# Kernel tuning notes

Hardware: AMD Instinct MI355X
Metric: run time of the kernel (lower is better)

## Reference

```python
import jax, jax.numpy as jnp
import numpy as np

R_BLOCKS = 8  # r: number of diagonal blocks

def _rotate(Wp, R):
    # Wp: [out, in], R: [r, b, b] with in = r*b.
    # Equivalent to Wp @ block_diag(R[0],...,R[r-1]) without materializing [in,in].
    o = Wp.shape[0]
    r, b, _ = R.shape
    Wb = Wp.reshape(o, r, b)
    return jnp.einsum('ori,rij->orj', Wb, R).reshape(o, r * b)

def setup_inputs() -> dict:
    key = jax.random.key(0)
    ks = jax.random.split(key, 6)
    in_f, out_f, r = 1024, 1024, R_BLOCKS
    blk = in_f // r
    return {
        'attn': jax.random.normal(ks[0], (3 * out_f, in_f), jnp.float32) * 0.02,
        'bias': jax.random.normal(ks[1], (3 * out_f,), jnp.float32) * 0.02,
        'x': jax.random.normal(ks[2], (4, 2048, in_f), jnp.float32),
        'q_R': jax.random.normal(ks[3], (r, blk, blk), jnp.float32) * 0.02,
        'k_R': jax.random.normal(ks[4], (r, blk, blk), jnp.float32) * 0.02,
        'v_R': jax.random.normal(ks[5], (r, blk, blk), jnp.float32) * 0.02,
    }

def reference(attn, bias, x, q_R, k_R, v_R):
    # attn.data in torch detaches the frozen pretrained weight
    W = jax.lax.stop_gradient(attn)
    Wq, Wk, Wv = jnp.split(W, 3, axis=0)
    filt = jnp.concatenate([_rotate(Wq, q_R), _rotate(Wk, k_R), _rotate(Wv, v_R)], axis=0)
    # F.linear: x @ filt.T + bias -> [B, S, 3*out]
    return jnp.einsum('bsi,oi->bso', x, filt) + bias
```

## Files before the change

### kernel.cpp

```cpp
#include <hip/hip_runtime.h>
#include <hip/hip_bf16.h>
#include <stdint.h>

typedef __attribute__((ext_vector_type(8))) short short8;
typedef __attribute__((ext_vector_type(4))) float floatx4;

#define M_TOT 8192
#define N_TOT 3072
#define K_TOT 1024

__device__ inline unsigned short f2bf(float f) {
    union { float f; unsigned int ui; } v; v.f = f;
    unsigned int x = v.ui;
    unsigned int r = (x + 0x7fffu + ((x >> 16) & 1u)) >> 16;
    return (unsigned short)r;
}

__device__ inline void gl2lds16(const void* g, void* l) {
    __builtin_amdgcn_global_load_lds(
        (__attribute__((address_space(1))) void*)g,
        (__attribute__((address_space(3))) void*)l,
        16, 0, 0);
}

__global__ __launch_bounds__(256) void cvt_f32_bf16_kernel(
    const float* __restrict__ in, unsigned short* __restrict__ out, int n8)
{
    int i = blockIdx.x * 256 + threadIdx.x;
    if (i >= n8) return;
    const float4* p = (const float4*)in + (size_t)i * 2;
    float4 a = p[0], b = p[1];
    short8 s;
    s[0] = (short)f2bf(a.x); s[1] = (short)f2bf(a.y);
    s[2] = (short)f2bf(a.z); s[3] = (short)f2bf(a.w);
    s[4] = (short)f2bf(b.x); s[5] = (short)f2bf(b.y);
    s[6] = (short)f2bf(b.z); s[7] = (short)f2bf(b.w);
    *(short8*)(out + (size_t)i * 8) = s;
}

__global__ __launch_bounds__(256) void rotate_w_kernel(
    const float* __restrict__ W,
    const float* __restrict__ qR,
    const float* __restrict__ kR,
    const float* __restrict__ vR,
    unsigned short* __restrict__ Fout)
{
    __shared__ float Rs[128 * 128];
    __shared__ float Ws[64 * 132];

    const int tid = threadIdx.x;
    const int o0 = blockIdx.x * 64;
    const int r = blockIdx.y;

    const float* R = (o0 < 1024) ? qR : (o0 < 2048) ? kR : vR;
    R += (size_t)r * 128 * 128;

#pragma unroll
    for (int i = 0; i < 16; ++i) {
        int idx = (i * 256 + tid) * 4;
        *(float4*)(Rs + idx) = *(const float4*)(R + idx);
    }
#pragma unroll
    for (int i = 0; i < 8; ++i) {
        int idx = (i * 256 + tid) * 4;
        int row = idx >> 7;
        int col = idx & 127;
        *(float4*)(Ws + row * 132 + col) =
            *(const float4*)(W + (size_t)(o0 + row) * K_TOT + r * 128 + col);
    }
    __syncthreads();

    const int jg = (tid & 15) * 8;
    const int ob = tid >> 4;

    float acc[4][8];
#pragma unroll
    for (int a = 0; a < 4; ++a)
#pragma unroll
        for (int b = 0; b < 8; ++b) acc[a][b] = 0.f;

    for (int i = 0; i < 128; ++i) {
        float4 r0 = *(const float4*)(Rs + i * 128 + jg);
        float4 r1 = *(const float4*)(Rs + i * 128 + jg + 4);
        float rv[8] = {r0.x, r0.y, r0.z, r0.w, r1.x, r1.y, r1.z, r1.w};
#pragma unroll
        for (int oo = 0; oo < 4; ++oo) {
            float wv = Ws[(ob + oo * 16) * 132 + i];
#pragma unroll
            for (int t = 0; t < 8; ++t) acc[oo][t] += wv * rv[t];
        }
    }

#pragma unroll
    for (int oo = 0; oo < 4; ++oo) {
        int o = o0 + ob + oo * 16;
        short8 s;
#pragma unroll
        for (int t = 0; t < 8; ++t) s[t] = (short)f2bf(acc[oo][t]);
        *(short8*)(Fout + (size_t)o * K_TOT + r * 128 + jg) = s;
    }
}

#define GKT 16

__global__ __launch_bounds__(512, 2) void gemm256_kernel(
    const unsigned short* __restrict__ X,
    const unsigned short* __restrict__ F,
    const float* __restrict__ bias,
    float* __restrict__ out)
{
    extern __shared__ unsigned short sm[];

    const int tid = threadIdx.x;
    const int wid = tid >> 6;
    const int l   = tid & 63;
    const int wm  = wid >> 2;
    const int wn  = wid & 3;

    const int bswz = (blockIdx.x & 7) * 48 + (blockIdx.x >> 3);
    const int m0 = (bswz / 12) * 256;
    const int n0 = (bswz % 12) * 256;

    const int srow  = tid >> 3;
    const int scb   = tid & 7;
    const int sgcb  = scb ^ (srow & 7);
    const int sswap = (tid >> 8) << 5;

    const unsigned short* Xs = X + (size_t)(m0 + srow) * K_TOT + sgcb * 8;
    const unsigned short* Fs = F + (size_t)(n0 + srow + sswap) * K_TOT + sgcb * 8;
    unsigned short* smA = sm + srow * 64 + scb * 8;
    unsigned short* smB = sm + 32768 + (srow + sswap) * 64 + scb * 8;

#define STAGE_A(bo, rb, kc) gl2lds16(Xs + (size_t)(rb) * K_TOT + (kc), smA + (bo) + (rb) * 64)
#define STAGE_B(bo, rb, kc) gl2lds16(Fs + (size_t)(rb) * K_TOT + (kc), smB + (bo) + (rb) * 64)
#define STAGE_Ag0(bo, kc) { STAGE_A(bo, 0, kc);  STAGE_A(bo, 128, kc); }
#define STAGE_Ag1(bo, kc) { STAGE_A(bo, 64, kc); STAGE_A(bo, 192, kc); }
#define STAGE_Bg0(bo, kc) { STAGE_B(bo, 0, kc);  STAGE_B(bo, 128, kc); }
#define STAGE_Bg1(bo, kc) { STAGE_B(bo, 32, kc); STAGE_B(bo, 160, kc); }
#define BARRIER() asm volatile("s_barrier" ::: "memory")

    const int l15 = l & 15;
    const int s8a = (((l >> 4) + 0) ^ (l & 7)) * 8;
    const int s8b = (((l >> 4) + 4) ^ (l & 7)) * 8;
    const int paBase = (wm * 128 + l15) * 64;
    const int pbBase = (wn * 64 + l15) * 64;

    floatx4 acc[8][4];
#pragma unroll
    for (int i = 0; i < 8; ++i)
#pragma unroll
        for (int j = 0; j < 4; ++j)
#pragma unroll
            for (int t = 0; t < 4; ++t) acc[i][j][t] = 0.f;

    short8 aF[4][2];
    short8 bF[2][2][2];

#define RD_A(QM, co) { _Pragma("unroll") for (int mf = 0; mf < 4; ++mf) { \
        const unsigned short* p = sm + (co) + paBase + ((QM) * 4 + mf) * 1024; \
        aF[mf][0] = *(const short8*)(p + s8a); \
        aF[mf][1] = *(const short8*)(p + s8b); } }
#define RD_B(QN, co) { _Pragma("unroll") for (int nf = 0; nf < 2; ++nf) { \
        const unsigned short* p = sm + 32768 + (co) + pbBase + ((QN) * 2 + nf) * 1024; \
        bF[QN][nf][0] = *(const short8*)(p + s8a); \
        bF[QN][nf][1] = *(const short8*)(p + s8b); } }
#define DO_MFMA(QM, QN) { __builtin_amdgcn_s_setprio(1); \
        _Pragma("unroll") for (int mf = 0; mf < 4; ++mf) \
        _Pragma("unroll") for (int nf = 0; nf < 2; ++nf) { \
            acc[(QM)*4+mf][(QN)*2+nf] = __builtin_amdgcn_mfma_f32_16x16x32_bf16( \
                aF[mf][0], bF[QN][nf][0], acc[(QM)*4+mf][(QN)*2+nf], 0, 0, 0); \
            acc[(QM)*4+mf][(QN)*2+nf] = __builtin_amdgcn_mfma_f32_16x16x32_bf16( \
                aF[mf][1], bF[QN][nf][1], acc[(QM)*4+mf][(QN)*2+nf], 0, 0, 0); } \
        __builtin_amdgcn_s_setprio(0); }

    STAGE_Ag0(0, 0); STAGE_Bg0(0, 0); STAGE_Bg1(0, 0); STAGE_Ag1(0, 0);
    STAGE_Ag0(16384, 64); STAGE_Bg0(16384, 64);
    asm volatile("s_waitcnt vmcnt(4)" ::: "memory");
    BARRIER();

    for (int kt = 0; kt < GKT; ++kt) {
        const int co = (kt & 1) << 14;
        const int no = co ^ 16384;
        const int kc1 = (kt + 1) * 64;
        const int kc2 = (kt + 2) * 64;

        RD_A(0, co); RD_B(0, co);
        if (kt + 1 < GKT) { STAGE_Bg1(no, kc1); }
        BARRIER();
        DO_MFMA(0, 0);
        BARRIER();

        RD_B(1, co);
        if (kt + 1 < GKT) { STAGE_Ag1(no, kc1); }
        BARRIER();
        DO_MFMA(0, 1);
        BARRIER();

        RD_A(1, co);
        if (kt + 2 < GKT) { STAGE_Ag0(co, kc2); }
        BARRIER();
        DO_MFMA(1, 0);
        BARRIER();

        if (kt + 2 < GKT) { STAGE_Bg0(co, kc2); }
        if (kt < GKT - 2) { asm volatile("s_waitcnt vmcnt(4)" ::: "memory"); }
        else              { asm volatile("s_waitcnt vmcnt(0)" ::: "memory"); }
        BARRIER();
        DO_MFMA(1, 1);
        BARRIER();
    }

    float bv[4];
#pragma unroll
    for (int nf = 0; nf < 4; ++nf) bv[nf] = bias[n0 + wn * 64 + nf * 16 + l15];

    const int mrow = m0 + wm * 128 + (l >> 4) * 4;
    const int ncol = n0 + wn * 64 + l15;
#pragma unroll
    for (int mf = 0; mf < 8; ++mf)
#pragma unroll
        for (int nf = 0; nf < 4; ++nf) {
            float* po = out + (size_t)(mrow + mf * 16) * N_TOT + ncol + nf * 16;
#pragma unroll
            for (int r = 0; r < 4; ++r)
                po[(size_t)r * N_TOT] = acc[mf][nf][r] + bv[nf];
        }
}

extern "C" void kernel_launch(void* const* d_in, const int* in_sizes, int n_in,
                              void* d_out, int out_size, void* d_ws, size_t ws_size,
                              hipStream_t stream) {
    const float* attn = (const float*)d_in[0];
    const float* bias = (const float*)d_in[1];
    const float* x    = (const float*)d_in[2];
    const float* qR   = (const float*)d_in[3];
    const float* kR   = (const float*)d_in[4];
    const float* vR   = (const float*)d_in[5];

    float* out = (float*)d_out;

    unsigned short* xb   = (unsigned short*)d_ws;
    unsigned short* filt = xb + (size_t)M_TOT * K_TOT;

    static bool attr_set = false;
    if (!attr_set) {
        hipFuncSetAttribute((const void*)gemm256_kernel,
                            hipFuncAttributeMaxDynamicSharedMemorySize, 131072);
        attr_set = true;
    }

    const int n8 = (M_TOT * K_TOT) / 8;
    cvt_f32_bf16_kernel<<<n8 / 256, 256, 0, stream>>>(x, xb, n8);
    rotate_w_kernel<<<dim3(48, 8), 256, 0, stream>>>(attn, qR, kR, vR, filt);
    gemm256_kernel<<<dim3(384), dim3(512), 131072, stream>>>(xb, filt, bias, out);
}
```

Measured before the change: 214.5 us.

## Restructure GEMM main loop into K-half phases with reordered LDS staging

Reorganizes the 256x256 bf16 GEMM inner loop so that each phase reads one K-half (s8a or s8b) of A for a quarter of the M fragments plus all four B fragments. MFMAs are then issued over 4x4 fragments per phase instead of 4x2 with two K steps. The global-to-LDS staging schedule is reordered to match: A1 is prefetched early, A0/B0/B1 for tile k+2 are issued later, and the wait threshold moves to vmcnt(6). The loop is manually unrolled by two with explicit tail tiles. The goal is better overlap of LDS reads and global prefetch with MFMA work and fewer register-file hazards, at the cost of holding more B fragments live.

Measured after the change: 215.2 us. About the same (+0.3%).

```diff
diff --git a/kernel.cpp b/kernel.cpp
--- a/kernel.cpp
+++ b/kernel.cpp
@@ -121,23 +121,25 @@
     const int m0 = (bswz / 12) * 256;
     const int n0 = (bswz % 12) * 256;
 
-    const int srow  = tid >> 3;
-    const int scb   = tid & 7;
-    const int sgcb  = scb ^ (srow & 7);
-    const int sswap = (tid >> 8) << 5;
+    const int srow = tid >> 3;
+    const int scb  = tid & 7;
+    const int sgcb = scb ^ (srow & 7);
 
     const unsigned short* Xs = X + (size_t)(m0 + srow) * K_TOT + sgcb * 8;
-    const unsigned short* Fs = F + (size_t)(n0 + srow + sswap) * K_TOT + sgcb * 8;
+    const unsigned short* Fs = F + (size_t)(n0 + srow) * K_TOT + sgcb * 8;
     unsigned short* smA = sm + srow * 64 + scb * 8;
-    unsigned short* smB = sm + 32768 + (srow + sswap) * 64 + scb * 8;
-
-#define STAGE_A(bo, rb, kc) gl2lds16(Xs + (size_t)(rb) * K_TOT + (kc), smA + (bo) + (rb) * 64)
-#define STAGE_B(bo, rb, kc) gl2lds16(Fs + (size_t)(rb) * K_TOT + (kc), smB + (bo) + (rb) * 64)
-#define STAGE_Ag0(bo, kc) { STAGE_A(bo, 0, kc);  STAGE_A(bo, 128, kc); }
-#define STAGE_Ag1(bo, kc) { STAGE_A(bo, 64, kc); STAGE_A(bo, 192, kc); }
-#define STAGE_Bg0(bo, kc) { STAGE_B(bo, 0, kc);  STAGE_B(bo, 128, kc); }
-#define STAGE_Bg1(bo, kc) { STAGE_B(bo, 32, kc); STAGE_B(bo, 160, kc); }
+    unsigned short* smB = sm + 32768 + srow * 64 + scb * 8;
+
+#define ST_A(bo, rb, kc) gl2lds16(Xs + (size_t)(rb) * K_TOT + (kc), smA + (bo) + (rb) * 64)
+#define ST_B(bo, rb, kc) gl2lds16(Fs + (size_t)(rb) * K_TOT + (kc), smB + (bo) + (rb) * 64)
+#define ST_A0(bo, kc) { ST_A(bo, 0, kc);   ST_A(bo, 128, kc); }
+#define ST_A1(bo, kc) { ST_A(bo, 64, kc);  ST_A(bo, 192, kc); }
+#define ST_B0(bo, kc) { ST_B(bo, 0, kc);   ST_B(bo, 64, kc);  }
+#define ST_B1(bo, kc) { ST_B(bo, 128, kc); ST_B(bo, 192, kc); }
 #define BARRIER() asm volatile("s_barrier" ::: "memory")
+#define VM6 asm volatile("s_waitcnt vmcnt(6)" ::: "memory")
+#define VM0 asm volatile("s_waitcnt vmcnt(0)" ::: "memory")
+#define VMNONE ((void)0)
 
     const int l15 = l & 15;
     const int s8a = (((l >> 4) + 0) ^ (l & 7)) * 8;
@@ -153,62 +155,51 @@
 #pragma unroll
             for (int t = 0; t < 4; ++t) acc[i][j][t] = 0.f;
 
-    short8 aF[4][2];
-    short8 bF[2][2][2];
-
-#define RD_A(QM, co) { _Pragma("unroll") for (int mf = 0; mf < 4; ++mf) { \
-        const unsigned short* p = sm + (co) + paBase + ((QM) * 4 + mf) * 1024; \
-        aF[mf][0] = *(const short8*)(p + s8a); \
-        aF[mf][1] = *(const short8*)(p + s8b); } }
-#define RD_B(QN, co) { _Pragma("unroll") for (int nf = 0; nf < 2; ++nf) { \
-        const unsigned short* p = sm + 32768 + (co) + pbBase + ((QN) * 2 + nf) * 1024; \
-        bF[QN][nf][0] = *(const short8*)(p + s8a); \
-        bF[QN][nf][1] = *(const short8*)(p + s8b); } }
-#define DO_MFMA(QM, QN) { __builtin_amdgcn_s_setprio(1); \
+    short8 aF[4];
+    short8 bF0[4];
+    short8 bF1[4];
+
+#define RD_AQ(QM, CO, SS) { _Pragma("unroll") for (int mf = 0; mf < 4; ++mf) \
+        aF[mf] = *(const short8*)(sm + (CO) + paBase + ((QM) * 4 + mf) * 1024 + (SS)); }
+#define RD_BK(DST, CO, SS) { _Pragma("unroll") for (int nf = 0; nf < 4; ++nf) \
+        DST[nf] = *(const short8*)(sm + 32768 + (CO) + pbBase + nf * 1024 + (SS)); }
+#define MFMA_Q(QM, BF) { __builtin_amdgcn_s_setprio(1); \
         _Pragma("unroll") for (int mf = 0; mf < 4; ++mf) \
-        _Pragma("unroll") for (int nf = 0; nf < 2; ++nf) { \
-            acc[(QM)*4+mf][(QN)*2+nf] = __builtin_amdgcn_mfma_f32_16x16x32_bf16( \
-                aF[mf][0], bF[QN][nf][0], acc[(QM)*4+mf][(QN)*2+nf], 0, 0, 0); \
-            acc[(QM)*4+mf][(QN)*2+nf] = __builtin_amdgcn_mfma_f32_16x16x32_bf16( \
-                aF[mf][1], bF[QN][nf][1], acc[(QM)*4+mf][(QN)*2+nf], 0, 0, 0); } \
+        _Pragma("unroll") for (int nf = 0; nf < 4; ++nf) \
+            acc[(QM) * 4 + mf][nf] = __builtin_amdgcn_mfma_f32_16x16x32_bf16( \
+                aF[mf], BF[nf], acc[(QM) * 4 + mf][nf], 0, 0, 0); \
         __builtin_amdgcn_s_setprio(0); }
 
-    STAGE_Ag0(0, 0); STAGE_Bg0(0, 0); STAGE_Bg1(0, 0); STAGE_Ag1(0, 0);
-    STAGE_Ag0(16384, 64); STAGE_Bg0(16384, 64);
-    asm volatile("s_waitcnt vmcnt(4)" ::: "memory");
+#define TILE(CO, NO, kc1, kc2, S1, S2, WN) { \
+         \
+        RD_AQ(0, CO, s8a); RD_BK(bF0, CO, s8a); \
+        if (S1) { ST_A1(NO, kc1); } \
+        BARRIER(); MFMA_Q(0, bF0); BARRIER(); \
+         \
+        RD_AQ(0, CO, s8b); RD_BK(bF1, CO, s8b); \
+        BARRIER(); MFMA_Q(0, bF1); BARRIER(); \
+         \
+        RD_AQ(1, CO, s8a); \
+        if (S2) { ST_A0(CO, kc2); ST_B0(CO, kc2); } \
+        BARRIER(); MFMA_Q(1, bF0); BARRIER(); \
+         \
+        RD_AQ(1, CO, s8b); \
+        if (S2) { ST_B1(CO, kc2); } \
+        WN; \
+        BARRIER(); MFMA_Q(1, bF1); BARRIER(); }
+
+    ST_A0(0, 0); ST_A1(0, 0); ST_B0(0, 0); ST_B1(0, 0);
+    ST_A0(16384, 64); ST_B0(16384, 64); ST_B1(16384, 64);
+    VM6;
     BARRIER();
 
-    for (int kt = 0; kt < GKT; ++kt) {
-        const int co = (kt & 1) << 14;
-        const int no = co ^ 16384;
-        const int kc1 = (kt + 1) * 64;
-        const int kc2 = (kt + 2) * 64;
-
-        RD_A(0, co); RD_B(0, co);
-        if (kt + 1 < GKT) { STAGE_Bg1(no, kc1); }
-        BARRIER();
-        DO_MFMA(0, 0);
-        BARRIER();
-
-        RD_B(1, co);
-        if (kt + 1 < GKT) { STAGE_Ag1(no, kc1); }
-        BARRIER();
-        DO_MFMA(0, 1);
-        BARRIER();
-
-        RD_A(1, co);
-        if (kt + 2 < GKT) { STAGE_Ag0(co, kc2); }
-        BARRIER();
-        DO_MFMA(1, 0);
-        BARRIER();
-
-        if (kt + 2 < GKT) { STAGE_Bg0(co, kc2); }
-        if (kt < GKT - 2) { asm volatile("s_waitcnt vmcnt(4)" ::: "memory"); }
-        else              { asm volatile("s_waitcnt vmcnt(0)" ::: "memory"); }
-        BARRIER();
-        DO_MFMA(1, 1);
-        BARRIER();
-    }
+    for (int kt2 = 0; kt2 < 7; ++kt2) {
+        const int k0 = kt2 * 128;
+        TILE(0,     16384, k0 + 64,  k0 + 128, 1, 1, VM6);
+        TILE(16384, 0,     k0 + 128, k0 + 192, 1, 1, VM6);
+    }
+    TILE(0,     16384, 960, 0, 1, 0, VM0);
+    TILE(16384, 0,     0,   0, 0, 0, VMNONE);
 
     float bv[4];
 #pragma unroll
```
